# Performance work log

Hardware: AMD Instinct MI355X
Metric: run time of the kernel (lower is better)

## Reference

```python
import jax, jax.numpy as jnp
import numpy as np

B, S, H, L = 64, 512, 768, 9


def setup_inputs() -> dict:
    key = jax.random.key(0)
    k0, k1, k2, k3, k4, k5, k6 = jax.random.split(key, 7)
    hidden = jax.random.normal(k0, (B, S, H), dtype=jnp.float32)
    W = jax.random.normal(k1, (L, H), dtype=jnp.float32) * 0.02
    b = jnp.zeros((L,), dtype=jnp.float32)
    start_transitions = jax.random.uniform(k2, (L,), minval=-0.1, maxval=0.1)
    end_transitions = jax.random.uniform(k3, (L,), minval=-0.1, maxval=0.1)
    transitions = jax.random.uniform(k4, (L, L), minval=-0.1, maxval=0.1)
    # variable-length sequences (position 0 always valid), like real padded batches
    lens = jax.random.randint(k5, (B,), S // 2, S + 1)
    attention_mask = jnp.arange(S)[None, :] < lens[:, None]  # (B,S) bool
    labels = jax.random.randint(k6, (B, S), 0, L).astype(jnp.int32)
    return dict(hidden=hidden, W=W, b=b, start_transitions=start_transitions,
                end_transitions=end_transitions, transitions=transitions,
                labels=labels, attention_mask=attention_mask)


def _crf_neg_log_likelihood(feats, labels, mask, start, end, trans):
    """feats (B,S,L) emissions; labels (B,S) int; mask (B,S) bool. Returns scalar mean NLL."""
    fdt = feats.dtype
    # ---- log denominator: forward algorithm as a scan over time ----
    fT = jnp.swapaxes(feats, 0, 1)  # (S,B,L)
    mT = jnp.swapaxes(mask, 0, 1)   # (S,B)
    alpha0 = start + fT[0]          # (B,L)

    def step(alpha, xs):
        f_t, m_t = xs
        # (B,L_prev,1) + (L_prev,L_next) + (B,1,L_next) -> logsumexp over prev
        new = jax.nn.logsumexp(alpha[:, :, None] + trans[None, :, :] + f_t[:, None, :], axis=1)
        return jnp.where(m_t[:, None], new, alpha), None

    alpha, _ = jax.lax.scan(step, alpha0, (fT[1:], mT[1:]))
    log_den = jax.nn.logsumexp(alpha + end, axis=1)  # (B,)

    # ---- log numerator: score of the gold path, fully vectorized ----
    emit = jnp.take_along_axis(feats, labels[..., None].astype(jnp.int32), axis=2)[..., 0]  # (B,S)
    tr = trans[labels[:, :-1], labels[:, 1:]]  # (B,S-1)
    score = start[labels[:, 0]] + emit[:, 0]
    score = score + jnp.sum((tr + emit[:, 1:]) * mask[:, 1:].astype(fdt), axis=1)
    lens = jnp.sum(mask.astype(jnp.int32), axis=1) - 1  # index of last valid token
    last_tags = jnp.take_along_axis(labels, lens[:, None], axis=1)[:, 0]
    score = score + end[last_tags]

    return jnp.mean(log_den - score)


def reference(hidden, W, b, start_transitions, end_transitions, transitions, labels, attention_mask):
    # hidden2label linear (dropout is identity in eval mode)
    feats = jnp.einsum('bsh,lh->bsl', hidden, W) + b  # (B,S,L)
    return _crf_neg_log_likelihood(feats, labels, attention_mask,
                                   start_transitions, end_transitions, transitions)
```

## Files before the change

kernel.cpp:

```cpp
#include <hip/hip_runtime.h>
#include <hip/hip_bf16.h>

#define BB 64
#define SS 512
#define HH 768
#define LL 9
#define CL 16
#define NC (SS / CL)
#define NEG (-1e30f)

#define EXP2F(x) exp2f(x)
#define LOG2F(x) __log2f(x)

static __device__ __forceinline__ float dot4(float4 a, float4 b) {
    return a.x * b.x + a.y * b.y + a.z * b.z + a.w * b.w;
}

static __device__ __forceinline__ float max9(const float* v) {
    float m1 = fmaxf(fmaxf(v[0], v[1]), v[2]);
    float m2 = fmaxf(fmaxf(v[3], v[4]), v[5]);
    float m3 = fmaxf(fmaxf(v[6], v[7]), v[8]);
    return fmaxf(fmaxf(m1, m2), m3);
}

static __device__ __forceinline__ float sum9exp(const float* v, float mx) {
    float e0 = EXP2F(v[0] - mx), e1 = EXP2F(v[1] - mx), e2 = EXP2F(v[2] - mx);
    float e3 = EXP2F(v[3] - mx), e4 = EXP2F(v[4] - mx), e5 = EXP2F(v[5] - mx);
    float e6 = EXP2F(v[6] - mx), e7 = EXP2F(v[7] - mx), e8 = EXP2F(v[8] - mx);
    return ((e0 + e1) + (e2 + e3)) + (((e4 + e5) + (e6 + e7)) + e8);
}

template <int CTRL>
static __device__ __forceinline__ float dpp_add(float v) {
    return v + __int_as_float(
        __builtin_amdgcn_update_dpp(0, __float_as_int(v), CTRL, 0xF, 0xF, true));
}

static __device__ __forceinline__ float wave_sum64(float v) {
    v = dpp_add<0xB1>(v);
    v = dpp_add<0x4E>(v);
    v = dpp_add<0x124>(v);
    v = dpp_add<0x128>(v);
    v += __shfl_xor(v, 16);
    v += __shfl_xor(v, 32);
    return v;
}

__global__ __launch_bounds__(256, 2)
void feats_kernel(const float* __restrict__ hidden,
                  const float* __restrict__ W,
                  const float* __restrict__ bias,
                  float* __restrict__ feats,
                  float* __restrict__ out0) {
    if (blockIdx.x == 0 && threadIdx.x == 0) out0[0] = 0.f;

    const int lane = threadIdx.x & 63;
    const int wv   = threadIdx.x >> 6;
    const int gw   = blockIdx.x * 4 + wv;
    const int nw   = 4096;

    float4 wreg[3][LL];
#pragma unroll
    for (int c = 0; c < 3; ++c)
#pragma unroll
        for (int l = 0; l < LL; ++l)
            wreg[c][l] = *(const float4*)(W + l * HH + c * 256 + (lane << 2));

    const float bv = bias[lane < LL ? lane : 0];

    for (int r0 = gw; r0 < BB * SS; r0 += 2 * nw) {
        const int r1 = r0 + nw;
        const float4* h0p = (const float4*)(hidden + (size_t)r0 * HH);
        const float4* h1p = (const float4*)(hidden + (size_t)r1 * HH);
        float4 a0 = h0p[lane], a1 = h0p[64 + lane], a2 = h0p[128 + lane];
        float4 b0 = h1p[lane], b1 = h1p[64 + lane], b2 = h1p[128 + lane];

        float accA[LL], accB[LL];
#pragma unroll
        for (int l = 0; l < LL; ++l) {
            accA[l] = dot4(a0, wreg[0][l]) + dot4(a1, wreg[1][l]) + dot4(a2, wreg[2][l]);
            accB[l] = dot4(b0, wreg[0][l]) + dot4(b1, wreg[1][l]) + dot4(b2, wreg[2][l]);
        }
        float outA = 0.f, outB = 0.f;
#pragma unroll
        for (int l = 0; l < LL; ++l) {
            float sA = wave_sum64(accA[l]);
            float sB = wave_sum64(accB[l]);
            if (lane == l) { outA = sA; outB = sB; }
        }
        if (lane < LL) {
            feats[(size_t)r0 * LL + lane] = outA + bv;
            feats[(size_t)r1 * LL + lane] = outB + bv;
        }
    }
}

__global__ __launch_bounds__(192, 6)
void crf_chunk_kernel(const float* __restrict__ feats,
                      const float* __restrict__ trans,
                      const int* __restrict__ mask,
                      float* __restrict__ Q) {
    __shared__ float Pb[2][12][16];
    const float INV_LN2 = 1.4426950408889634f;
    const int b   = blockIdx.x / NC;
    const int c   = blockIdx.x % NC;
    const int tid = threadIdx.x;
    const int i   = tid >> 4;
    const int j   = tid & 15;
    const int jc  = j < LL ? j : LL - 1;

    float trC[LL];
#pragma unroll
    for (int k = 0; k < LL; ++k) trC[k] = trans[k * LL + jc] * INV_LN2;

    const int t0    = (c == 0) ? 1 : c * CL;
    const int steps = (c + 1) * CL - t0;

    const float* fb = feats + (size_t)b * SS * LL;
    const int*   mb = mask + b * SS;

    float fs[CL];
    int   na = 0;
#pragma unroll
    for (int s = 0; s < CL; ++s) {
        if (s < steps) {
            const int t = t0 + s;
            fs[s] = fb[t * LL + jc] * INV_LN2;
            na += (mb[t] != 0) ? 1 : 0;
        } else {
            fs[s] = 0.f;
        }
    }

    float P = (i == j) ? 0.f : NEG;
    Pb[0][i][j] = P;
    __syncthreads();

#pragma unroll
    for (int s = 0; s < CL; ++s) {
        if (s < na) {
            const float* row = &Pb[s & 1][i][0];
            float v[LL];
#pragma unroll
            for (int k = 0; k < LL; ++k) v[k] = row[k] + trC[k];
            const float mx  = max9(v);
            const float sum = sum9exp(v, mx);
            P = mx + LOG2F(sum) + fs[s];
            Pb[(s + 1) & 1][i][j] = P;
        }
        __syncthreads();
    }

    if (i < LL && j < LL)
        Q[((size_t)(b * NC + c)) * (LL * LL) + i * LL + j] = P;
}

__global__ __launch_bounds__(64, 1)
void crf_combine_kernel(const float* __restrict__ feats,
                        const float* __restrict__ Q,
                        const float* __restrict__ start_t,
                        const float* __restrict__ end_t,
                        const float* __restrict__ trans,
                        const int* __restrict__ labels,
                        const int* __restrict__ mask,
                        float* __restrict__ out) {
    const int b    = blockIdx.x;
    const int lane = threadIdx.x;
    const int j    = lane < LL ? lane : LL - 1;
    const float INV_LN2 = 1.4426950408889634f;
    const float LN2     = 0.6931471805599453f;

    const float* fb = feats + (size_t)b * SS * LL;
    const int*   lb = labels + b * SS;
    const int*   mb = mask + b * SS;
    const float* Qb = Q + (size_t)b * NC * (LL * LL);

    float partial = 0.f;
    int   cnt     = 0;
    for (int t = lane; t < SS; t += 64) {
        const int m = mb[t];
        cnt += (m != 0);
        if (t >= 1 && m) {
            const int lp = lb[t - 1], lc = lb[t];
            partial += trans[lp * LL + lc] + fb[t * LL + lc];
        }
    }
#pragma unroll
    for (int off = 1; off < 64; off <<= 1) {
        partial += __shfl_xor(partial, off);
        cnt     += __shfl_xor(cnt, off);
    }

    float alpha[LL];
#pragma unroll
    for (int k = 0; k < LL; ++k) alpha[k] = (start_t[k] + fb[k]) * INV_LN2;

    float qcol[LL], qnext[LL];
#pragma unroll
    for (int k = 0; k < LL; ++k) qnext[k] = Qb[k * LL + j];
    for (int c = 0; c < NC; ++c) {
#pragma unroll
        for (int k = 0; k < LL; ++k) qcol[k] = qnext[k];
        if (c + 1 < NC) {
            const float* Qn = Qb + (size_t)(c + 1) * (LL * LL);
#pragma unroll
            for (int k = 0; k < LL; ++k) qnext[k] = Qn[k * LL + j];
        }
        float v[LL];
#pragma unroll
        for (int k = 0; k < LL; ++k) v[k] = alpha[k] + qcol[k];
        const float mx  = max9(v);
        const float sum = sum9exp(v, mx);
        const float anew = mx + LOG2F(sum);
#pragma unroll
        for (int k = 0; k < LL; ++k)
            alpha[k] = __uint_as_float(__builtin_amdgcn_readlane(__float_as_uint(anew), k));
    }

    float v[LL];
#pragma unroll
    for (int k = 0; k < LL; ++k) v[k] = alpha[k] + end_t[k] * INV_LN2;
    const float mx  = max9(v);
    const float sum = sum9exp(v, mx);
    const float log_den = (mx + LOG2F(sum)) * LN2;

    if (lane == 0) {
        const int l0 = lb[0];
        const float score = start_t[l0] + fb[l0] + partial + end_t[lb[cnt - 1]];
        atomicAdd(out, (log_den - score) * (1.0f / BB));
    }
}

extern "C" void kernel_launch(void* const* d_in, const int* in_sizes, int n_in,
                              void* d_out, int out_size, void* d_ws, size_t ws_size,
                              hipStream_t stream) {
    const float* hidden = (const float*)d_in[0];
    const float* W      = (const float*)d_in[1];
    const float* bias   = (const float*)d_in[2];
    const float* startT = (const float*)d_in[3];
    const float* endT   = (const float*)d_in[4];
    const float* trans  = (const float*)d_in[5];
    const int*   labels = (const int*)d_in[6];
    const int*   mask   = (const int*)d_in[7];

    float* feats = (float*)d_ws;
    float* Q     = feats + (size_t)BB * SS * LL;

    feats_kernel<<<dim3(1024), dim3(256), 0, stream>>>(hidden, W, bias, feats, (float*)d_out);
    crf_chunk_kernel<<<dim3(BB * NC), dim3(192), 0, stream>>>(feats, trans, mask, Q);
    crf_combine_kernel<<<dim3(BB), dim3(64), 0, stream>>>(feats, Q, startT, endT, trans,
                                                          labels, mask, (float*)d_out);
}
```

Baseline: 203.4 us.

## Fuse emission projection with per-chunk CRF transfer and gold-path scoring

Merges the feature projection and the per-chunk CRF matrix-product kernel into one kernel: each block computes the 16 emission rows of its chunk into shared memory, then runs the chunk's log-semiring recurrence and a per-chunk gold-path score. The combine kernel now only reduces the per-chunk scores and runs the alpha recurrence over chunk matrices. This removes the feats round trip through global memory and one kernel launch. The cost is a per-chunk serial recurrence inside the heavy GEMV blocks, which may reduce overlap of memory streaming.

```diff
diff --git a/kernel.cpp b/kernel.cpp
--- a/kernel.cpp
+++ b/kernel.cpp
@@ -47,34 +47,77 @@
 }
 
 __global__ __launch_bounds__(256, 2)
-void feats_kernel(const float* __restrict__ hidden,
+void fused_kernel(const float* __restrict__ hidden,
                   const float* __restrict__ W,
                   const float* __restrict__ bias,
-                  float* __restrict__ feats,
+                  const float* __restrict__ start_t,
+                  const float* __restrict__ end_t,
+                  const float* __restrict__ trans,
+                  const int* __restrict__ labels,
+                  const int* __restrict__ mask,
+                  float* __restrict__ Q,
+                  float* __restrict__ A0,
+                  float* __restrict__ Sc,
                   float* __restrict__ out0) {
-    if (blockIdx.x == 0 && threadIdx.x == 0) out0[0] = 0.f;
-
-    const int lane = threadIdx.x & 63;
-    const int wv   = threadIdx.x >> 6;
-    const int gw   = blockIdx.x * 4 + wv;
-    const int nw   = 4096;
+    const int bid  = blockIdx.x;
+    const int b    = bid >> 5;
+    const int c    = bid & (NC - 1);
+    const int tid  = threadIdx.x;
+    const int lane = tid & 63;
+    const int wv   = tid >> 6;
+
+    if (bid == 0 && tid == 0) out0[0] = 0.f;
+
+    __shared__ float fsl[CL][12];
+    __shared__ float Pb[2][LL][16];
+
+    const int bS     = b * SS;
+    const int t_base = c * CL;
+
+    const int i  = tid >> 4;
+    const int j  = tid & 15;
+    const int jc = j < LL ? j : LL - 1;
+    const float INV_LN2 = 1.4426950408889634f;
+
+    float trC[LL];
+#pragma unroll
+    for (int k = 0; k < LL; ++k) trC[k] = trans[k * LL + jc] * INV_LN2;
+
+    const int off   = (c == 0) ? 1 : 0;
+    const int steps = CL - off;
+    const int t0    = t_base + off;
+
+    int na = 0;
+#pragma unroll
+    for (int u = 0; u < CL; ++u)
+        na += (u < steps && mask[bS + t0 + u] != 0) ? 1 : 0;
+
+    int mt = 0, lc = 0, lp = 0, mnext = 0;
+    const int t_sc = t_base + lane;
+    if (wv == 3 && lane < CL) {
+        mt    = mask[bS + t_sc];
+        lc    = labels[bS + t_sc];
+        lp    = (t_sc >= 1) ? labels[bS + t_sc - 1] : 0;
+        mnext = (t_sc == SS - 1) ? 0 : mask[bS + t_sc + 1];
+    }
 
     float4 wreg[3][LL];
 #pragma unroll
-    for (int c = 0; c < 3; ++c)
+    for (int c3 = 0; c3 < 3; ++c3)
 #pragma unroll
         for (int l = 0; l < LL; ++l)
-            wreg[c][l] = *(const float4*)(W + l * HH + c * 256 + (lane << 2));
-
+            wreg[c3][l] = *(const float4*)(W + l * HH + c3 * 256 + (lane << 2));
     const float bv = bias[lane < LL ? lane : 0];
 
-    for (int r0 = gw; r0 < BB * SS; r0 += 2 * nw) {
-        const int r1 = r0 + nw;
-        const float4* h0p = (const float4*)(hidden + (size_t)r0 * HH);
-        const float4* h1p = (const float4*)(hidden + (size_t)r1 * HH);
+    const float* hbase = hidden + ((size_t)bS + t_base) * HH;
+#pragma unroll
+    for (int pair = 0; pair < 2; ++pair) {
+        const int r0 = wv * 4 + pair * 2;
+        const int r1 = r0 + 1;
+        const float4* h0p = (const float4*)(hbase + (size_t)r0 * HH);
+        const float4* h1p = (const float4*)(hbase + (size_t)r1 * HH);
         float4 a0 = h0p[lane], a1 = h0p[64 + lane], a2 = h0p[128 + lane];
         float4 b0 = h1p[lane], b1 = h1p[64 + lane], b2 = h1p[128 + lane];
-
         float accA[LL], accB[LL];
 #pragma unroll
         for (int l = 0; l < LL; ++l) {
@@ -89,120 +132,82 @@
             if (lane == l) { outA = sA; outB = sB; }
         }
         if (lane < LL) {
-            feats[(size_t)r0 * LL + lane] = outA + bv;
-            feats[(size_t)r1 * LL + lane] = outB + bv;
-        }
-    }
-}
-
-__global__ __launch_bounds__(192, 6)
-void crf_chunk_kernel(const float* __restrict__ feats,
-                      const float* __restrict__ trans,
-                      const int* __restrict__ mask,
-                      float* __restrict__ Q) {
-    __shared__ float Pb[2][12][16];
-    const float INV_LN2 = 1.4426950408889634f;
-    const int b   = blockIdx.x / NC;
-    const int c   = blockIdx.x % NC;
-    const int tid = threadIdx.x;
-    const int i   = tid >> 4;
-    const int j   = tid & 15;
-    const int jc  = j < LL ? j : LL - 1;
-
-    float trC[LL];
-#pragma unroll
-    for (int k = 0; k < LL; ++k) trC[k] = trans[k * LL + jc] * INV_LN2;
-
-    const int t0    = (c == 0) ? 1 : c * CL;
-    const int steps = (c + 1) * CL - t0;
-
-    const float* fb = feats + (size_t)b * SS * LL;
-    const int*   mb = mask + b * SS;
-
-    float fs[CL];
-    int   na = 0;
-#pragma unroll
-    for (int s = 0; s < CL; ++s) {
-        if (s < steps) {
-            const int t = t0 + s;
-            fs[s] = fb[t * LL + jc] * INV_LN2;
-            na += (mb[t] != 0) ? 1 : 0;
-        } else {
-            fs[s] = 0.f;
+            fsl[r0][lane] = outA + bv;
+            fsl[r1][lane] = outB + bv;
         }
     }
 
     float P = (i == j) ? 0.f : NEG;
-    Pb[0][i][j] = P;
+    if (tid < 144) Pb[0][i][j] = P;
     __syncthreads();
+
+    if (wv == 3 && lane < CL) {
+        float sc = 0.f;
+        if (t_sc >= 1 && mt) sc += trans[lp * LL + lc] + fsl[lane][lc];
+        if (t_sc == 0)       sc += start_t[lc] + fsl[0][lc];
+        if (mt && !mnext)    sc += end_t[lc];
+#pragma unroll
+        for (int o = 1; o < CL; o <<= 1) sc += __shfl_xor(sc, o);
+        if (lane == 0) Sc[bid] = sc;
+        if (c == 0 && lane < LL)
+            A0[b * 16 + lane] = (start_t[lane] + fsl[0][lane]) * INV_LN2;
+    }
+
+    float fsr[CL];
+#pragma unroll
+    for (int u = 0; u < CL; ++u)
+        fsr[u] = (u < steps) ? fsl[u + off][jc] * INV_LN2 : 0.f;
 
 #pragma unroll
     for (int s = 0; s < CL; ++s) {
         if (s < na) {
-            const float* row = &Pb[s & 1][i][0];
-            float v[LL];
-#pragma unroll
-            for (int k = 0; k < LL; ++k) v[k] = row[k] + trC[k];
-            const float mx  = max9(v);
-            const float sum = sum9exp(v, mx);
-            P = mx + LOG2F(sum) + fs[s];
-            Pb[(s + 1) & 1][i][j] = P;
+            if (tid < 144) {
+                const float* row = &Pb[s & 1][i][0];
+                float v[LL];
+#pragma unroll
+                for (int k = 0; k < LL; ++k) v[k] = row[k] + trC[k];
+                const float mx  = max9(v);
+                const float sum = sum9exp(v, mx);
+                P = mx + LOG2F(sum) + fsr[s];
+                Pb[(s + 1) & 1][i][j] = P;
+            }
         }
         __syncthreads();
     }
 
-    if (i < LL && j < LL)
-        Q[((size_t)(b * NC + c)) * (LL * LL) + i * LL + j] = P;
+    if (tid < 144 && j < LL)
+        Q[(size_t)bid * (LL * LL) + i * LL + j] = P;
 }
 
 __global__ __launch_bounds__(64, 1)
-void crf_combine_kernel(const float* __restrict__ feats,
-                        const float* __restrict__ Q,
-                        const float* __restrict__ start_t,
-                        const float* __restrict__ end_t,
-                        const float* __restrict__ trans,
-                        const int* __restrict__ labels,
-                        const int* __restrict__ mask,
-                        float* __restrict__ out) {
+void combine_kernel(const float* __restrict__ Q,
+                    const float* __restrict__ A0,
+                    const float* __restrict__ Sc,
+                    const float* __restrict__ end_t,
+                    float* __restrict__ out) {
     const int b    = blockIdx.x;
     const int lane = threadIdx.x;
     const int j    = lane < LL ? lane : LL - 1;
     const float INV_LN2 = 1.4426950408889634f;
     const float LN2     = 0.6931471805599453f;
 
-    const float* fb = feats + (size_t)b * SS * LL;
-    const int*   lb = labels + b * SS;
-    const int*   mb = mask + b * SS;
+    float score = (lane < NC) ? Sc[b * NC + lane] : 0.f;
+#pragma unroll
+    for (int o = 1; o < 64; o <<= 1) score += __shfl_xor(score, o);
+
+    float alpha[LL];
+#pragma unroll
+    for (int k = 0; k < LL; ++k) alpha[k] = A0[b * 16 + k];
+
     const float* Qb = Q + (size_t)b * NC * (LL * LL);
-
-    float partial = 0.f;
-    int   cnt     = 0;
-    for (int t = lane; t < SS; t += 64) {
-        const int m = mb[t];
-        cnt += (m != 0);
-        if (t >= 1 && m) {
-            const int lp = lb[t - 1], lc = lb[t];
-            partial += trans[lp * LL + lc] + fb[t * LL + lc];
-        }
-    }
-#pragma unroll
-    for (int off = 1; off < 64; off <<= 1) {
-        partial += __shfl_xor(partial, off);
-        cnt     += __shfl_xor(cnt, off);
-    }
-
-    float alpha[LL];
-#pragma unroll
-    for (int k = 0; k < LL; ++k) alpha[k] = (start_t[k] + fb[k]) * INV_LN2;
-
     float qcol[LL], qnext[LL];
 #pragma unroll
     for (int k = 0; k < LL; ++k) qnext[k] = Qb[k * LL + j];
-    for (int c = 0; c < NC; ++c) {
+    for (int cc = 0; cc < NC; ++cc) {
 #pragma unroll
         for (int k = 0; k < LL; ++k) qcol[k] = qnext[k];
-        if (c + 1 < NC) {
-            const float* Qn = Qb + (size_t)(c + 1) * (LL * LL);
+        if (cc + 1 < NC) {
+            const float* Qn = Qb + (size_t)(cc + 1) * (LL * LL);
 #pragma unroll
             for (int k = 0; k < LL; ++k) qnext[k] = Qn[k * LL + j];
         }
@@ -224,11 +229,8 @@
     const float sum = sum9exp(v, mx);
     const float log_den = (mx + LOG2F(sum)) * LN2;
 
-    if (lane == 0) {
-        const int l0 = lb[0];
-        const float score = start_t[l0] + fb[l0] + partial + end_t[lb[cnt - 1]];
+    if (lane == 0)
         atomicAdd(out, (log_den - score) * (1.0f / BB));
-    }
 }
 
 extern "C" void kernel_launch(void* const* d_in, const int* in_sizes, int n_in,
@@ -243,11 +245,11 @@
     const int*   labels = (const int*)d_in[6];
     const int*   mask   = (const int*)d_in[7];
 
-    float* feats = (float*)d_ws;
-    float* Q     = feats + (size_t)BB * SS * LL;
-
-    feats_kernel<<<dim3(1024), dim3(256), 0, stream>>>(hidden, W, bias, feats, (float*)d_out);
-    crf_chunk_kernel<<<dim3(BB * NC), dim3(192), 0, stream>>>(feats, trans, mask, Q);
-    crf_combine_kernel<<<dim3(BB), dim3(64), 0, stream>>>(feats, Q, startT, endT, trans,
-                                                          labels, mask, (float*)d_out);
-}
+    float* Q  = (float*)d_ws;
+    float* A0 = Q + (size_t)BB * NC * LL * LL;
+    float* Sc = A0 + BB * 16;
+
+    fused_kernel<<<dim3(BB * NC), dim3(256), 0, stream>>>(
+        hidden, W, bias, startT, endT, trans, labels, mask, Q, A0, Sc, (float*)d_out);
+    combine_kernel<<<dim3(BB), dim3(64), 0, stream>>>(Q, A0, Sc, endT, (float*)d_out);
+}
```

Result: faster. 192.3 us (-5.4%).
